# Optimization experiments

Hardware: AMD Instinct MI355X
Metric: run time of the kernel (lower is better)

## Reference

```python
import jax, jax.numpy as jnp
import numpy as np

B, S, P, N, V = 8, 16, 32, 2048, 2562
K_SAMPLE = 500      # samples_per_slot
K_NEAREST = 3
MIN_DIST = 0.5
FALLOFF = 5.0
GW, SW, RW = 0.7, 0.3, 0.2


def _icosphere(level=4):
    t = (1.0 + 5.0 ** 0.5) / 2.0
    v = np.array([[-1, t, 0], [1, t, 0], [-1, -t, 0], [1, -t, 0],
                  [0, -1, t], [0, 1, t], [0, -1, -t], [0, 1, -t],
                  [t, 0, -1], [t, 0, 1], [-t, 0, -1], [-t, 0, 1]], dtype=np.float64)
    v /= np.linalg.norm(v, axis=1, keepdims=True)
    f = [[0, 11, 5], [0, 5, 1], [0, 1, 7], [0, 7, 10], [0, 10, 11],
         [1, 5, 9], [5, 11, 4], [11, 10, 2], [10, 7, 6], [7, 1, 8],
         [3, 9, 4], [3, 4, 2], [3, 2, 6], [3, 6, 8], [3, 8, 9],
         [4, 9, 5], [2, 4, 11], [6, 2, 10], [8, 6, 7], [9, 8, 1]]
    verts = [x for x in v]
    for _ in range(level):
        cache = {}
        def mid(a, b):
            key = (min(a, b), max(a, b))
            if key in cache:
                return cache[key]
            m = verts[a] + verts[b]
            m = m / np.linalg.norm(m)
            verts.append(m)
            cache[key] = len(verts) - 1
            return cache[key]
        nf = []
        for a, b, c in f:
            ab, bc, ca = mid(a, b), mid(b, c), mid(c, a)
            nf += [[a, ab, ca], [b, bc, ab], [c, ca, bc], [ab, bc, ca]]
        f = nf
    return np.asarray(verts, dtype=np.float32)


def _euler_xyz_to_matrix(ang):
    # pytorch3d euler_angles_to_matrix(..., 'XYZ'): R = Rx(a) @ Ry(b) @ Rz(c)
    a, b, c = ang[..., 0], ang[..., 1], ang[..., 2]
    ca, sa = jnp.cos(a), jnp.sin(a)
    cb, sb = jnp.cos(b), jnp.sin(b)
    cc, sc = jnp.cos(c), jnp.sin(c)
    o, z = jnp.ones_like(a), jnp.zeros_like(a)
    sh = ang.shape[:-1] + (3, 3)
    Rx = jnp.stack([o, z, z, z, ca, -sa, z, sa, ca], -1).reshape(sh)
    Ry = jnp.stack([cb, z, sb, z, o, z, -sb, z, cb], -1).reshape(sh)
    Rz = jnp.stack([cc, -sc, z, sc, cc, z, z, z, o], -1).reshape(sh)
    return Rx @ Ry @ Rz


def _cdist2(x, y):
    # squared euclidean distances: x [..., n, 3], y [..., m, 3] -> [..., n, m]
    x2 = (x * x).sum(-1)[..., :, None]
    y2 = (y * y).sum(-1)[..., None, :]
    return jnp.maximum(x2 + y2 - 2.0 * jnp.einsum('...nd,...md->...nm', x, y), 0.0)


def _forward(scales, transforms, prototype_weights, prototype_offsets, target_pcl, verts):
    # --- transform_mesh ---
    R = _euler_xyz_to_matrix(transforms[..., 3:])          # [B,S,P,3,3]
    deformed = verts[None] + prototype_offsets              # [P,V,3]
    rotated = jnp.einsum('pvj,bspij->bspvi', deformed, R)   # verts @ R^T
    scaled = rotated * scales[:, :, None, None, :]          # [B,S,P,V,3]
    translated = scaled + transforms[:, :, :, None, :3]
    final = jnp.einsum('bspvi,bsp->bsvi', translated, prototype_weights)  # [B,S,V,3]

    # --- hybrid chamfer loss ---
    pred = final[:, :, :K_SAMPLE, :]                        # deterministic per-slot samples
    pred_flat = pred.reshape(B, S * K_SAMPLE, 3)
    # global: target -> all predicted points, mean of K nearest squared dists
    d2g = _cdist2(target_pcl, pred_flat)                    # [B,N,S*K]
    knn = -jax.lax.top_k(-d2g, K_NEAREST)[0]
    global_loss = knn.mean()
    # per-slot: each slot's points -> target, nearest neighbor squared dist
    d2s = _cdist2(pred, target_pcl[:, None])                # [B,S,K,N]
    per_slot_loss = d2s.min(-1).mean()
    # centroid repulsion
    cent = final.mean(axis=2)                               # [B,S,3]
    eye = jnp.eye(S, dtype=final.dtype)
    d = jnp.sqrt(_cdist2(cent, cent) + eye)                 # eye keeps diag grads finite
    rep = jnp.exp(FALLOFF * jnp.maximum(MIN_DIST - d, 0.0)) * (1.0 - eye)
    rep_loss = (rep.sum(axis=(1, 2)) / (S * (S - 1))).mean()

    return GW * global_loss + SW * per_slot_loss + RW * rep_loss


def setup_inputs() -> dict:
    key = jax.random.key(0)
    ks = jax.random.split(key, 5)
    scales = jax.random.uniform(ks[0], (B, S, 1), jnp.float32) * 0.5 + 0.5
    transforms = jax.random.normal(ks[1], (B, S, P, 6), jnp.float32)
    w = jax.random.uniform(ks[2], (B, S, P), jnp.float32) + 1e-3
    prototype_weights = w / w.sum(-1, keepdims=True)
    prototype_offsets = jax.random.normal(ks[3], (P, V, 3), jnp.float32) * 0.1
    target_pcl = jax.random.normal(ks[4], (B, N, 3), jnp.float32)
    verts = jnp.asarray(_icosphere(4))                      # [2562,3]
    return {"scales": scales, "transforms": transforms,
            "prototype_weights": prototype_weights,
            "prototype_offsets": prototype_offsets,
            "target_pcl": target_pcl, "verts": verts}


def reference(scales, transforms, prototype_weights, prototype_offsets, target_pcl, verts):
    return _forward(scales, transforms, prototype_weights, prototype_offsets, target_pcl, verts)
```

## Files before the change

### kernel.cpp

```cpp
#include <hip/hip_runtime.h>
#include <math.h>

namespace {
constexpr int cB = 8, cS = 16, cP = 32, cN = 2048, cV = 2562;
constexpr int cK = 500;
constexpr int cJ = cS * cK;
constexpr int cJC = 64;
constexpr int cJCH = cJ / cJC;
constexpr int cNC = 16;
constexpr int cNCH = cN / cNC;
constexpr int cJPAD = 8192;
constexpr int cBN = cB * cN;
constexpr float FINF = 3.402823466e+38f;

constexpr int OFF_PRED4 = 0;
constexpr int OFF_TGT4  = 256000;
constexpr int OFF_VBAR  = 321536;
constexpr int OFF_OBAR  = 321540;
constexpr int OFF_SM    = 321664;
constexpr int OFF_SC    = 358528;
constexpr int OFF_T3    = 358912;
constexpr int OFF_PSP   = 3504640;
constexpr int OFF_GM    = 4553216;
constexpr int OFF_PS    = 4553280;
}

__device__ __forceinline__ float block_sum(float v, float* red, int tid) {
  red[tid] = v;
  __syncthreads();
  for (int s = 128; s > 0; s >>= 1) {
    if (tid < s) red[tid] += red[tid + s];
    __syncthreads();
  }
  return red[0];
}

__device__ __forceinline__ void top3_insert(float& t0, float& t1, float& t2, float d) {
  const float n1 = __builtin_amdgcn_fmed3f(t0, t1, d);
  const float n2 = __builtin_amdgcn_fmed3f(t1, t2, d);
  t0 = fminf(t0, d);
  t1 = n1;
  t2 = n2;
}

__global__ void __launch_bounds__(256) k_front(const float* __restrict__ scales,
                                               const float* __restrict__ transforms,
                                               const float* __restrict__ pw,
                                               const float* __restrict__ offs,
                                               const float* __restrict__ verts,
                                               const float* __restrict__ target,
                                               float* __restrict__ ws) {
  const int blk = blockIdx.x;
  const int tid = threadIdx.x;
  if (blk <= cP) {
    __shared__ float red[256];
    const float* src = (blk < cP) ? (offs + blk * cV * 3) : verts;
    float acc0 = 0.f, acc1 = 0.f, acc2 = 0.f;
    for (int v = tid; v < cV; v += 256) {
      acc0 += src[v * 3 + 0];
      acc1 += src[v * 3 + 1];
      acc2 += src[v * 3 + 2];
    }
    float* dst = (blk < cP) ? (ws + OFF_OBAR + blk * 3) : (ws + OFF_VBAR);
    float a[3] = {acc0, acc1, acc2};
    for (int c = 0; c < 3; ++c) {
      float s = block_sum(a[c], red, tid);
      if (tid == 0) dst[c] = s / (float)cV;
      __syncthreads();
    }
  } else if (blk <= cP + 64) {
    const int idx = (blk - (cP + 1)) * 256 + tid;
    const float x = target[idx * 3 + 0];
    const float y = target[idx * 3 + 1];
    const float z = target[idx * 3 + 2];
    ((float4*)(ws + OFF_TGT4))[idx] =
        make_float4(x, y, z, 0.5f * fmaf(x, x, fmaf(y, y, z * z)));
  } else {
    const int bs = blk - (cP + 65);
    __shared__ float sM[cP][9];
    __shared__ float sC[3];
    __shared__ float sWT[cP][3];
    if (tid < cP) {
      const int p = tid;
      const float* t = transforms + (bs * cP + p) * 6;
      const float w = pw[bs * cP + p];
      const float sc = scales[bs];
      const float a = t[3], b = t[4], c = t[5];
      const float ca = cosf(a), sa = sinf(a);
      const float cb = cosf(b), sb = sinf(b);
      const float cg = cosf(c), sg = sinf(c);
      const float f = w * sc;
      sM[p][0] = f * (cb * cg);
      sM[p][1] = f * (-cb * sg);
      sM[p][2] = f * (sb);
      sM[p][3] = f * (ca * sg + sa * sb * cg);
      sM[p][4] = f * (ca * cg - sa * sb * sg);
      sM[p][5] = f * (-sa * cb);
      sM[p][6] = f * (sa * sg - ca * sb * cg);
      sM[p][7] = f * (sa * cg + ca * sb * sg);
      sM[p][8] = f * (ca * cb);
      sWT[p][0] = w * t[0];
      sWT[p][1] = w * t[1];
      sWT[p][2] = w * t[2];
    }
    __syncthreads();
    if (tid < 3) {
      float s = 0.f;
      for (int p = 0; p < cP; ++p) s += sWT[p][tid];
      sC[tid] = s;
    }
    __syncthreads();
    if (tid < cP * 9) ws[OFF_SM + bs * 288 + tid] = ((const float*)sM)[tid];
    if (tid < 3) ws[OFF_SC + bs * 3 + tid] = sC[tid];
    for (int k = tid; k < cK; k += 256) {
      const float x0 = verts[k * 3 + 0], x1 = verts[k * 3 + 1], x2 = verts[k * 3 + 2];
      float a0 = sC[0], a1 = sC[1], a2 = sC[2];
#pragma unroll 8
      for (int p = 0; p < cP; ++p) {
        const float* o = offs + (p * cV + k) * 3;
        const float d0 = x0 + o[0], d1 = x1 + o[1], d2 = x2 + o[2];
        a0 = fmaf(sM[p][0], d0, fmaf(sM[p][1], d1, fmaf(sM[p][2], d2, a0)));
        a1 = fmaf(sM[p][3], d0, fmaf(sM[p][4], d1, fmaf(sM[p][5], d2, a1)));
        a2 = fmaf(sM[p][6], d0, fmaf(sM[p][7], d1, fmaf(sM[p][8], d2, a2)));
      }
      ((float4*)(ws + OFF_PRED4))[bs * cK + k] =
          make_float4(a0, a1, a2, 0.5f * fmaf(a0, a0, fmaf(a1, a1, a2 * a2)));
    }
  }
}

__global__ void __launch_bounds__(256, 4) k_dist(float* __restrict__ ws) {
  __shared__ float4 sBuf[cNCH];
  const int blk = blockIdx.x;
  const int tid = threadIdx.x;
  const int rnd = blk >> 8;
  const int lane = blk & 255;
  const int role = (lane + rnd) & 1;
  const int sub = rnd * 128 + (lane >> 1);
  if (role == 0) {
    const int b = sub & 7;
    const int jc = sub >> 3;
    const float4* pr = (const float4*)(ws + OFF_PRED4) + b * cJ + jc * cJCH;
    if (tid < cJCH) sBuf[tid] = pr[tid];
    __syncthreads();
    const float4* tg = (const float4*)(ws + OFF_TGT4) + b * cN;
    float4 t[8];
#pragma unroll
    for (int q = 0; q < 8; ++q) t[q] = tg[tid + q * 256];
    float a0[8], a1[8], a2[8];
#pragma unroll
    for (int q = 0; q < 8; ++q) { a0[q] = FINF; a1[q] = FINF; a2[q] = FINF; }
    for (int j = 0; j < cJCH; ++j) {
      const float4 p = sBuf[j];
#pragma unroll
      for (int q = 0; q < 8; ++q) {
        const float s =
            fmaf(-t[q].x, p.x, fmaf(-t[q].y, p.y, fmaf(-t[q].z, p.z, p.w)));
        top3_insert(a0[q], a1[q], a2[q], s);
      }
    }
    float* plane = ws + OFF_T3 + (jc * 3) * cBN;
#pragma unroll
    for (int q = 0; q < 8; ++q) {
      const int idx = b * cN + tid + q * 256;
      plane[0 * cBN + idx] = a0[q];
      plane[1 * cBN + idx] = a1[q];
      plane[2 * cBN + idx] = a2[q];
    }
  } else {
    const int jb = sub & 3;
    const int nc = (sub >> 2) & 15;
    const int b = sub >> 6;
    const float4* tg = (const float4*)(ws + OFF_TGT4) + b * cN + nc * cNCH;
    if (tid < cNCH) sBuf[tid] = tg[tid];
    __syncthreads();
    const float4* pr = (const float4*)(ws + OFF_PRED4) + b * cJ;
    float px[8], py[8], pz[8];
    float m[8] = {FINF, FINF, FINF, FINF, FINF, FINF, FINF, FINF};
#pragma unroll
    for (int q = 0; q < 8; ++q) {
      int j = jb * 2048 + q * 256 + tid;
      j = (j < cJ) ? j : (cJ - 1);
      const float4 p = pr[j];
      px[q] = p.x; py[q] = p.y; pz[q] = p.z;
    }
#pragma unroll 2
    for (int n = 0; n < cNCH; ++n) {
      const float4 t = sBuf[n];
#pragma unroll
      for (int q = 0; q < 8; ++q) {
        const float s = fmaf(-px[q], t.x, fmaf(-py[q], t.y, fmaf(-pz[q], t.z, t.w)));
        m[q] = fminf(m[q], s);
      }
    }
    float* o = ws + OFF_PSP + (b * cNC + nc) * cJPAD + jb * 2048 + tid;
#pragma unroll
    for (int q = 0; q < 8; ++q) o[q * 256] = m[q];
  }
}

__global__ void __launch_bounds__(256) k_merge(float* __restrict__ ws) {
  __shared__ float red[256];
  const int blk = blockIdx.x;
  const int tid = threadIdx.x;
  if (blk < 64) {
    const int idx = blk * 256 + tid;
    const float* plane = ws + OFF_T3;
    float t0 = FINF, t1 = FINF, t2 = FINF;
#pragma unroll 8
    for (int q = 0; q < cJC * 3; ++q)
      top3_insert(t0, t1, t2, plane[q * cBN + idx]);
    const float ht = ws[OFF_TGT4 + idx * 4 + 3];
    const float d0 = fmaxf(2.f * (t0 + ht), 0.f);
    const float d1 = fmaxf(2.f * (t1 + ht), 0.f);
    const float d2 = fmaxf(2.f * (t2 + ht), 0.f);
    const float s = block_sum(d0 + d1 + d2, red, tid);
    if (tid == 0) ws[OFF_GM + blk] = s;
  } else {
    const int rb = blk - 64;
    const int b = rb >> 5;
    const int jb = rb & 31;
    const int j = jb * 256 + tid;
    float contrib = 0.f;
    if (j < cJ) {
      float m = FINF;
#pragma unroll
      for (int nc = 0; nc < cNC; ++nc)
        m = fminf(m, ws[OFF_PSP + (b * cNC + nc) * cJPAD + j]);
      const float hp = ws[OFF_PRED4 + (b * cJ + j) * 4 + 3];
      contrib = fmaxf(2.f * (m + hp), 0.f);
    }
    const float s = block_sum(contrib, red, tid);
    if (tid == 0) ws[OFF_PS + b * 32 + jb] = s;
  }
}

__global__ void __launch_bounds__(256) k_final(float* __restrict__ ws, float* __restrict__ out) {
  __shared__ float red[256];
  __shared__ float scent[cB * cS * 3];
  const int tid = threadIdx.x;
  if (tid < cB * cS) {
    const int bs = tid;
    const float* M = ws + OFF_SM + bs * 288;
    const float* vb = ws + OFF_VBAR;
    float c0 = ws[OFF_SC + bs * 3 + 0];
    float c1 = ws[OFF_SC + bs * 3 + 1];
    float c2 = ws[OFF_SC + bs * 3 + 2];
#pragma unroll 8
    for (int p = 0; p < cP; ++p) {
      const float* ob = ws + OFF_OBAR + p * 3;
      const float d0 = vb[0] + ob[0], d1 = vb[1] + ob[1], d2 = vb[2] + ob[2];
      c0 = fmaf(M[p * 9 + 0], d0, fmaf(M[p * 9 + 1], d1, fmaf(M[p * 9 + 2], d2, c0)));
      c1 = fmaf(M[p * 9 + 3], d0, fmaf(M[p * 9 + 4], d1, fmaf(M[p * 9 + 5], d2, c1)));
      c2 = fmaf(M[p * 9 + 6], d0, fmaf(M[p * 9 + 7], d1, fmaf(M[p * 9 + 8], d2, c2)));
    }
    scent[bs * 3 + 0] = c0;
    scent[bs * 3 + 1] = c1;
    scent[bs * 3 + 2] = c2;
  }
  __syncthreads();
  float acc = 0.f;
  for (int idx = tid; idx < cB * cS * cS; idx += 256) {
    const int b = idx / (cS * cS);
    const int r = idx % (cS * cS);
    const int i = r / cS, jj = r % cS;
    if (i == jj) continue;
    const float* ci = scent + (b * cS + i) * 3;
    const float* cj = scent + (b * cS + jj) * 3;
    const float dx = ci[0] - cj[0], dy = ci[1] - cj[1], dz = ci[2] - cj[2];
    const float d = sqrtf(fmaf(dx, dx, fmaf(dy, dy, dz * dz)));
    acc += expf(5.0f * fmaxf(0.5f - d, 0.0f));
  }
  const float repsum = block_sum(acc, red, tid);
  __syncthreads();
  const float gsum = block_sum((tid < 64) ? ws[OFF_GM + tid] : 0.f, red, tid);
  __syncthreads();
  const float pssum = block_sum(ws[OFF_PS + tid], red, tid);
  if (tid == 0) {
    const float global_loss = gsum / (float)(cB * cN * 3);
    const float per_slot = pssum / (float)(cB * cS * cK);
    const float rep = repsum / (float)(cB * cS * (cS - 1));
    out[0] = 0.7f * global_loss + 0.3f * per_slot + 0.2f * rep;
  }
}

extern "C" void kernel_launch(void* const* d_in, const int* in_sizes, int n_in,
                              void* d_out, int out_size, void* d_ws, size_t ws_size,
                              hipStream_t stream) {
  const float* scales     = (const float*)d_in[0];
  const float* transforms = (const float*)d_in[1];
  const float* pw         = (const float*)d_in[2];
  const float* offs       = (const float*)d_in[3];
  const float* target     = (const float*)d_in[4];
  const float* verts      = (const float*)d_in[5];
  float* out = (float*)d_out;
  float* ws = (float*)d_ws;

  k_front<<<cP + 1 + 64 + cB * cS, 256, 0, stream>>>(scales, transforms, pw, offs,
                                                     verts, target, ws);
  k_dist<<<1024, 256, 0, stream>>>(ws);
  k_merge<<<64 + 256, 256, 0, stream>>>(ws);
  k_final<<<1, 256, 0, stream>>>(ws, out);
}
```

Measured before the change: 72.15 us.

## Compute pairwise distances with bf16 split-precision MFMA and fused bidirectional reductions

```diff
diff --git a/kernel.cpp b/kernel.cpp
--- a/kernel.cpp
+++ b/kernel.cpp
@@ -5,25 +5,23 @@
 constexpr int cB = 8, cS = 16, cP = 32, cN = 2048, cV = 2562;
 constexpr int cK = 500;
 constexpr int cJ = cS * cK;
-constexpr int cJC = 64;
-constexpr int cJCH = cJ / cJC;
-constexpr int cNC = 16;
-constexpr int cNCH = cN / cNC;
-constexpr int cJPAD = 8192;
-constexpr int cBN = cB * cN;
+constexpr int cJP = 8192;
 constexpr float FINF = 3.402823466e+38f;
 
-constexpr int OFF_PRED4 = 0;
-constexpr int OFF_TGT4  = 256000;
-constexpr int OFF_VBAR  = 321536;
-constexpr int OFF_OBAR  = 321540;
-constexpr int OFF_SM    = 321664;
-constexpr int OFF_SC    = 358528;
-constexpr int OFF_T3    = 358912;
-constexpr int OFF_PSP   = 3504640;
-constexpr int OFF_GM    = 4553216;
-constexpr int OFF_PS    = 4553280;
-}
+constexpr int OFF_TF   = 0;
+constexpr int OFF_PF   = 131072;
+constexpr int OFF_PSP  = 655360;
+constexpr int OFF_T3   = 2752512;
+constexpr int OFF_VBAR = 4849664;
+constexpr int OFF_OBAR = 4849668;
+constexpr int OFF_SM   = 4849792;
+constexpr int OFF_SC   = 4886656;
+constexpr int OFF_GM   = 4887040;
+constexpr int OFF_PS   = 4887104;
+}
+
+typedef __attribute__((ext_vector_type(8))) short bf16x8;
+typedef __attribute__((ext_vector_type(4))) float f32x4;
 
 __device__ __forceinline__ float block_sum(float v, float* red, int tid) {
   red[tid] = v;
@@ -41,6 +39,14 @@
   t0 = fminf(t0, d);
   t1 = n1;
   t2 = n2;
+}
+
+__device__ __forceinline__ unsigned short f2bf(float x) {
+  unsigned b = __float_as_uint(x);
+  return (unsigned short)((b + 0x7FFFu + ((b >> 16) & 1u)) >> 16);
+}
+__device__ __forceinline__ float bf2f(unsigned short u) {
+  return __uint_as_float(((unsigned)u) << 16);
 }
 
 __global__ void __launch_bounds__(256) k_front(const float* __restrict__ scales,
@@ -52,6 +58,7 @@
                                                float* __restrict__ ws) {
   const int blk = blockIdx.x;
   const int tid = threadIdx.x;
+  const unsigned short ONE = 0x3F80;
   if (blk <= cP) {
     __shared__ float red[256];
     const float* src = (blk < cP) ? (offs + blk * cV * 3) : verts;
@@ -73,10 +80,21 @@
     const float x = target[idx * 3 + 0];
     const float y = target[idx * 3 + 1];
     const float z = target[idx * 3 + 2];
-    ((float4*)(ws + OFF_TGT4))[idx] =
-        make_float4(x, y, z, 0.5f * fmaf(x, x, fmaf(y, y, z * z)));
-  } else {
+    const unsigned short thx = f2bf(x), thy = f2bf(y), thz = f2bf(z);
+    const unsigned short tlx = f2bf(x - bf2f(thx));
+    const unsigned short tly = f2bf(y - bf2f(thy));
+    const unsigned short tlz = f2bf(z - bf2f(thz));
+    const float ht = 0.5f * fmaf(x, x, fmaf(y, y, z * z));
+    const unsigned short hth = f2bf(ht);
+    const unsigned short htl = f2bf(ht - bf2f(hth));
+    unsigned short f[16] = {thx, thy, thz, thx, thy, thz, tlx, tly, tlz,
+                            ONE, ONE, hth, htl, 0, 0, 0};
+    float4* dst = (float4*)(ws + OFF_TF) + idx * 2;
+    dst[0] = *(const float4*)&f[0];
+    dst[1] = *(const float4*)&f[8];
+  } else if (blk <= cP + 64 + cB * cS) {
     const int bs = blk - (cP + 65);
+    const int b = bs >> 4, s = bs & 15;
     __shared__ float sM[cP][9];
     __shared__ float sC[3];
     __shared__ float sWT[cP][3];
@@ -85,9 +103,9 @@
       const float* t = transforms + (bs * cP + p) * 6;
       const float w = pw[bs * cP + p];
       const float sc = scales[bs];
-      const float a = t[3], b = t[4], c = t[5];
+      const float a = t[3], bb = t[4], c = t[5];
       const float ca = cosf(a), sa = sinf(a);
-      const float cb = cosf(b), sb = sinf(b);
+      const float cb = cosf(bb), sb = sinf(bb);
       const float cg = cosf(c), sg = sinf(c);
       const float f = w * sc;
       sM[p][0] = f * (cb * cg);
@@ -105,9 +123,9 @@
     }
     __syncthreads();
     if (tid < 3) {
-      float s = 0.f;
-      for (int p = 0; p < cP; ++p) s += sWT[p][tid];
-      sC[tid] = s;
+      float s2 = 0.f;
+      for (int p = 0; p < cP; ++p) s2 += sWT[p][tid];
+      sC[tid] = s2;
     }
     __syncthreads();
     if (tid < cP * 9) ws[OFF_SM + bs * 288 + tid] = ((const float*)sM)[tid];
@@ -123,79 +141,139 @@
         a1 = fmaf(sM[p][3], d0, fmaf(sM[p][4], d1, fmaf(sM[p][5], d2, a1)));
         a2 = fmaf(sM[p][6], d0, fmaf(sM[p][7], d1, fmaf(sM[p][8], d2, a2)));
       }
-      ((float4*)(ws + OFF_PRED4))[bs * cK + k] =
-          make_float4(a0, a1, a2, 0.5f * fmaf(a0, a0, fmaf(a1, a1, a2 * a2)));
-    }
-  }
-}
-
-__global__ void __launch_bounds__(256, 4) k_dist(float* __restrict__ ws) {
-  __shared__ float4 sBuf[cNCH];
+      const unsigned short phx = f2bf(a0), phy = f2bf(a1), phz = f2bf(a2);
+      const unsigned short plx = f2bf(a0 - bf2f(phx));
+      const unsigned short ply = f2bf(a1 - bf2f(phy));
+      const unsigned short plz = f2bf(a2 - bf2f(phz));
+      const float hp = 0.5f * fmaf(a0, a0, fmaf(a1, a1, a2 * a2));
+      const unsigned short hph = f2bf(hp);
+      const unsigned short hpl = f2bf(hp - bf2f(hph));
+      unsigned short f[16] = {
+          (unsigned short)(phx ^ 0x8000), (unsigned short)(phy ^ 0x8000),
+          (unsigned short)(phz ^ 0x8000), (unsigned short)(plx ^ 0x8000),
+          (unsigned short)(ply ^ 0x8000), (unsigned short)(plz ^ 0x8000),
+          (unsigned short)(phx ^ 0x8000), (unsigned short)(phy ^ 0x8000),
+          (unsigned short)(phz ^ 0x8000), hph, hpl, ONE, ONE, 0, 0, 0};
+      float4* dst = (float4*)(ws + OFF_PF) + (b * cJP + s * cK + k) * 2;
+      dst[0] = *(const float4*)&f[0];
+      dst[1] = *(const float4*)&f[8];
+    }
+  } else {
+    for (int i = tid; i < cB * (cJP - cJ); i += 256) {
+      const int b = i / (cJP - cJ);
+      const int j = cJ + i % (cJP - cJ);
+      unsigned short f[16] = {0};
+      f[9] = f2bf(30000.0f);
+      float4* dst = (float4*)(ws + OFF_PF) + (b * cJP + j) * 2;
+      dst[0] = *(const float4*)&f[0];
+      dst[1] = *(const float4*)&f[8];
+    }
+  }
+}
+
+__global__ void __launch_bounds__(256) k_distm(float* __restrict__ ws) {
+  __shared__ unsigned short sFrag[1024 * 16 + 16];
+  __shared__ float sMin[4][514];
   const int blk = blockIdx.x;
   const int tid = threadIdx.x;
-  const int rnd = blk >> 8;
-  const int lane = blk & 255;
-  const int role = (lane + rnd) & 1;
-  const int sub = rnd * 128 + (lane >> 1);
-  if (role == 0) {
-    const int b = sub & 7;
-    const int jc = sub >> 3;
-    const float4* pr = (const float4*)(ws + OFF_PRED4) + b * cJ + jc * cJCH;
-    if (tid < cJCH) sBuf[tid] = pr[tid];
-    __syncthreads();
-    const float4* tg = (const float4*)(ws + OFF_TGT4) + b * cN;
-    float4 t[8];
-#pragma unroll
-    for (int q = 0; q < 8; ++q) t[q] = tg[tid + q * 256];
-    float a0[8], a1[8], a2[8];
-#pragma unroll
-    for (int q = 0; q < 8; ++q) { a0[q] = FINF; a1[q] = FINF; a2[q] = FINF; }
-    for (int j = 0; j < cJCH; ++j) {
-      const float4 p = sBuf[j];
-#pragma unroll
-      for (int q = 0; q < 8; ++q) {
-        const float s =
-            fmaf(-t[q].x, p.x, fmaf(-t[q].y, p.y, fmaf(-t[q].z, p.z, p.w)));
-        top3_insert(a0[q], a1[q], a2[q], s);
+  const int e = blk & 7;
+  const int tg = (blk >> 3) & 15;
+  const int b = blk >> 7;
+  {
+    const float4* src = (const float4*)(ws + OFF_PF) + (b * cJP + e * 1024) * 2;
+    float4* dst = (float4*)sFrag;
+    for (int i = tid; i < 2048; i += 256) dst[i] = src[i];
+    if (tid < 16) sFrag[1024 * 16 + tid] = 0;
+  }
+  const int w = tid >> 6, lane = tid & 63;
+  const int lcol = lane & 15, lh = lane >> 4;
+  for (int i = lane; i < 512; i += 64) sMin[w][i] = FINF;
+  __syncthreads();
+
+  const int half = w >> 1;
+  const int tgBase = tg * 128 + (w & 1) * 64;
+  const f32x4 zf = {0.f, 0.f, 0.f, 0.f};
+  bf16x8 afr0, afr1, afr2, afr3;
+  {
+    const float4* tf = (const float4*)(ws + OFF_TF);
+    float4 z4 = make_float4(0.f, 0.f, 0.f, 0.f);
+    float4 v0 = z4, v1 = z4, v2 = z4, v3 = z4;
+    if (lh < 2) {
+      const int base = (b * cN + tgBase + lcol) * 2 + lh;
+      v0 = tf[base + 0 * 32];
+      v1 = tf[base + 1 * 32];
+      v2 = tf[base + 2 * 32];
+      v3 = tf[base + 3 * 32];
+    }
+    afr0 = __builtin_bit_cast(bf16x8, v0);
+    afr1 = __builtin_bit_cast(bf16x8, v1);
+    afr2 = __builtin_bit_cast(bf16x8, v2);
+    afr3 = __builtin_bit_cast(bf16x8, v3);
+  }
+  float T0[4][4], T1[4][4], T2[4][4];
+#pragma unroll
+  for (int m = 0; m < 4; ++m)
+#pragma unroll
+    for (int r = 0; r < 4; ++r) { T0[m][r] = FINF; T1[m][r] = FINF; T2[m][r] = FINF; }
+
+  int bidx = (lh < 2) ? ((half * 512 + lcol) * 16 + lh * 8) : (1024 * 16);
+  const int bstep = (lh < 2) ? 256 : 0;
+
+#pragma unroll 2
+  for (int t = 0; t < 32; ++t) {
+    const bf16x8 bfr = *(const bf16x8*)(&sFrag[bidx]);
+    bidx += bstep;
+    f32x4 c0 = __builtin_amdgcn_mfma_f32_16x16x32_bf16(afr0, bfr, zf, 0, 0, 0);
+    f32x4 c1 = __builtin_amdgcn_mfma_f32_16x16x32_bf16(afr1, bfr, zf, 0, 0, 0);
+    f32x4 c2 = __builtin_amdgcn_mfma_f32_16x16x32_bf16(afr2, bfr, zf, 0, 0, 0);
+    f32x4 c3 = __builtin_amdgcn_mfma_f32_16x16x32_bf16(afr3, bfr, zf, 0, 0, 0);
+#pragma unroll
+    for (int r = 0; r < 4; ++r) top3_insert(T0[0][r], T1[0][r], T2[0][r], c0[r]);
+#pragma unroll
+    for (int r = 0; r < 4; ++r) top3_insert(T0[1][r], T1[1][r], T2[1][r], c1[r]);
+#pragma unroll
+    for (int r = 0; r < 4; ++r) top3_insert(T0[2][r], T1[2][r], T2[2][r], c2[r]);
+#pragma unroll
+    for (int r = 0; r < 4; ++r) top3_insert(T0[3][r], T1[3][r], T2[3][r], c3[r]);
+    float v = fminf(fminf(fminf(c0[0], c0[1]), fminf(c0[2], c0[3])),
+                    fminf(fminf(c1[0], c1[1]), fminf(c1[2], c1[3])));
+    v = fminf(v, fminf(fminf(fminf(c2[0], c2[1]), fminf(c2[2], c2[3])),
+                       fminf(fminf(c3[0], c3[1]), fminf(c3[2], c3[3]))));
+    v = fminf(v, __shfl_xor(v, 16));
+    v = fminf(v, __shfl_xor(v, 32));
+    const int si = t * 16 + lcol;
+    sMin[w][si] = fminf(sMin[w][si], v);
+  }
+  {
+    const int slot = tg * 2 + (w & 1);
+    float* dst = ws + OFF_PSP + (b * 32 + slot) * cJP + e * 1024 + half * 512;
+    for (int i = lane; i < 512; i += 64) dst[i] = sMin[w][i];
+  }
+  for (int mask = 1; mask < 16; mask <<= 1) {
+#pragma unroll
+    for (int m = 0; m < 4; ++m)
+#pragma unroll
+      for (int r = 0; r < 4; ++r) {
+        const float y0 = __shfl_xor(T0[m][r], mask);
+        const float y1 = __shfl_xor(T1[m][r], mask);
+        const float y2 = __shfl_xor(T2[m][r], mask);
+        top3_insert(T0[m][r], T1[m][r], T2[m][r], y0);
+        top3_insert(T0[m][r], T1[m][r], T2[m][r], y1);
+        top3_insert(T0[m][r], T1[m][r], T2[m][r], y2);
       }
-    }
-    float* plane = ws + OFF_T3 + (jc * 3) * cBN;
-#pragma unroll
-    for (int q = 0; q < 8; ++q) {
-      const int idx = b * cN + tid + q * 256;
-      plane[0 * cBN + idx] = a0[q];
-      plane[1 * cBN + idx] = a1[q];
-      plane[2 * cBN + idx] = a2[q];
-    }
-  } else {
-    const int jb = sub & 3;
-    const int nc = (sub >> 2) & 15;
-    const int b = sub >> 6;
-    const float4* tg = (const float4*)(ws + OFF_TGT4) + b * cN + nc * cNCH;
-    if (tid < cNCH) sBuf[tid] = tg[tid];
-    __syncthreads();
-    const float4* pr = (const float4*)(ws + OFF_PRED4) + b * cJ;
-    float px[8], py[8], pz[8];
-    float m[8] = {FINF, FINF, FINF, FINF, FINF, FINF, FINF, FINF};
-#pragma unroll
-    for (int q = 0; q < 8; ++q) {
-      int j = jb * 2048 + q * 256 + tid;
-      j = (j < cJ) ? j : (cJ - 1);
-      const float4 p = pr[j];
-      px[q] = p.x; py[q] = p.y; pz[q] = p.z;
-    }
-#pragma unroll 2
-    for (int n = 0; n < cNCH; ++n) {
-      const float4 t = sBuf[n];
-#pragma unroll
-      for (int q = 0; q < 8; ++q) {
-        const float s = fmaf(-px[q], t.x, fmaf(-py[q], t.y, fmaf(-pz[q], t.z, t.w)));
-        m[q] = fminf(m[q], s);
+  }
+  if (lcol == 0) {
+    const int slice = e * 2 + half;
+#pragma unroll
+    for (int m = 0; m < 4; ++m)
+#pragma unroll
+      for (int r = 0; r < 4; ++r) {
+        const int tgt = tgBase + m * 16 + lh * 4 + r;
+        float* dst = ws + OFF_T3 + ((b * 16 + slice) * cN + tgt) * 4;
+        dst[0] = T0[m][r];
+        dst[1] = T1[m][r];
+        dst[2] = T2[m][r];
       }
-    }
-    float* o = ws + OFF_PSP + (b * cNC + nc) * cJPAD + jb * 2048 + tid;
-#pragma unroll
-    for (int q = 0; q < 8; ++q) o[q * 256] = m[q];
   }
 }
 
@@ -205,15 +283,18 @@
   const int tid = threadIdx.x;
   if (blk < 64) {
     const int idx = blk * 256 + tid;
-    const float* plane = ws + OFF_T3;
+    const int b = idx >> 11, n = idx & 2047;
     float t0 = FINF, t1 = FINF, t2 = FINF;
-#pragma unroll 8
-    for (int q = 0; q < cJC * 3; ++q)
-      top3_insert(t0, t1, t2, plane[q * cBN + idx]);
-    const float ht = ws[OFF_TGT4 + idx * 4 + 3];
-    const float d0 = fmaxf(2.f * (t0 + ht), 0.f);
-    const float d1 = fmaxf(2.f * (t1 + ht), 0.f);
-    const float d2 = fmaxf(2.f * (t2 + ht), 0.f);
+#pragma unroll
+    for (int e = 0; e < 16; ++e) {
+      const float* src = ws + OFF_T3 + ((b * 16 + e) * cN + n) * 4;
+      top3_insert(t0, t1, t2, src[0]);
+      top3_insert(t0, t1, t2, src[1]);
+      top3_insert(t0, t1, t2, src[2]);
+    }
+    const float d0 = fmaxf(2.f * t0, 0.f);
+    const float d1 = fmaxf(2.f * t1, 0.f);
+    const float d2 = fmaxf(2.f * t2, 0.f);
     const float s = block_sum(d0 + d1 + d2, red, tid);
     if (tid == 0) ws[OFF_GM + blk] = s;
   } else {
@@ -225,10 +306,9 @@
     if (j < cJ) {
       float m = FINF;
 #pragma unroll
-      for (int nc = 0; nc < cNC; ++nc)
-        m = fminf(m, ws[OFF_PSP + (b * cNC + nc) * cJPAD + j]);
-      const float hp = ws[OFF_PRED4 + (b * cJ + j) * 4 + 3];
-      contrib = fmaxf(2.f * (m + hp), 0.f);
+      for (int s = 0; s < 32; ++s)
+        m = fminf(m, ws[OFF_PSP + (b * 32 + s) * cJP + j]);
+      contrib = fmaxf(2.f * m, 0.f);
     }
     const float s = block_sum(contrib, red, tid);
     if (tid == 0) ws[OFF_PS + b * 32 + jb] = s;
@@ -296,9 +376,9 @@
   float* out = (float*)d_out;
   float* ws = (float*)d_ws;
 
-  k_front<<<cP + 1 + 64 + cB * cS, 256, 0, stream>>>(scales, transforms, pw, offs,
-                                                     verts, target, ws);
-  k_dist<<<1024, 256, 0, stream>>>(ws);
+  k_front<<<cP + 1 + 64 + cB * cS + 1, 256, 0, stream>>>(scales, transforms, pw, offs,
+                                                         verts, target, ws);
+  k_distm<<<1024, 256, 0, stream>>>(ws);
   k_merge<<<64 + 256, 256, 0, stream>>>(ws);
   k_final<<<1, 256, 0, stream>>>(ws, out);
 }
```

Measured after the change: 69.25 us. -4.0%, faster.
